# Kernel tuning notes

Measured on AMD Instinct MI355X. Metric: run time of the kernel, lower is better.

## Reference

```python
import jax, jax.numpy as jnp
import numpy as np

N_HEADS = 16


def setup_inputs() -> dict:
    key = jax.random.key(0)
    ks = jax.random.split(key, 5)
    B, S, L, E, H = 8, 2048, 512, 1024, 1024
    x = jax.random.normal(ks[0], (B, S, E), dtype=jnp.float32)
    latents = jax.random.normal(ks[1], (B, L, E), dtype=jnp.float32)
    mask_x = jnp.ones((B, S), dtype=jnp.float32)
    mask_latent = jnp.ones((B, L), dtype=jnp.float32)
    # torch Linear(in, out, bias=False) stores W as [out, in] and computes x @ W.T;
    # we store [in, out] so forward is x @ W. Scale like torch default init.
    Wq = jax.random.normal(ks[2], (E, H), dtype=jnp.float32) / np.sqrt(E)
    Wkv = jax.random.normal(ks[3], (E, 2 * H), dtype=jnp.float32) / np.sqrt(E)
    Wp = jax.random.normal(ks[4], (H, E), dtype=jnp.float32) / np.sqrt(H)
    return {"x": x, "latents": latents, "mask_x": mask_x,
            "mask_latent": mask_latent, "Wq": Wq, "Wkv": Wkv, "Wp": Wp}


def reference(x, latents, mask_x, mask_latent, Wq, Wkv, Wp):
    B, L, E = latents.shape
    H = Wq.shape[1]
    d = H // N_HEADS

    q = latents @ Wq                                  # [B, L, H]
    kv_input = jnp.concatenate((x, latents), axis=1)  # [B, S+L, E]
    kv_mask = jnp.concatenate((mask_x, mask_latent), axis=1)  # [B, S+L]
    kv = kv_input @ Wkv                               # [B, S+L, 2H]
    k, v = kv[..., :H], kv[..., H:]

    def heads(t):  # [B, T, H] -> [B, nh, T, d]
        return t.reshape(t.shape[0], t.shape[1], N_HEADS, d).transpose(0, 2, 1, 3)

    q, k, v = heads(q), heads(k), heads(v)

    scores = jnp.einsum('bhld,bhsd->bhls', q, k) / jnp.sqrt(jnp.asarray(d, q.dtype))
    # additive padding mask: (1 - q_mask*kv_mask) * finfo.min, broadcast over heads
    m = mask_latent[:, None, :, None] * kv_mask[:, None, None, :]  # [B,1,L,S+L]
    scores = scores + (1.0 - m) * jnp.finfo(scores.dtype).min
    attn = jax.nn.softmax(scores, axis=-1)            # dropout is identity (eval)

    y = jnp.einsum('bhls,bhsd->bhld', attn, v)        # [B, nh, L, d]
    y = y.transpose(0, 2, 1, 3).reshape(B, L, H)
    return y @ Wp                                     # [B, L, E]
```

## Files before the change

kernel.cpp:

```cpp
#include <hip/hip_runtime.h>
#include <stdint.h>

typedef unsigned short u16;
typedef __attribute__((ext_vector_type(8))) short short8;
typedef __attribute__((ext_vector_type(4))) float f32x4;
typedef __attribute__((ext_vector_type(16))) float f32x16;
typedef __attribute__((ext_vector_type(4))) unsigned short u16x4;

__device__ __forceinline__ u16 f2bf(float f) {
  uint32_t u = __float_as_uint(f);
  return (u16)((u + 0x7FFFu + ((u >> 16) & 1u)) >> 16);
}

__device__ __forceinline__ void gl2lds16(const u16* g, u16* l) {
  __builtin_amdgcn_global_load_lds(
      (const __attribute__((address_space(1))) unsigned int*)g,
      (__attribute__((address_space(3))) unsigned int*)l, 16, 0, 0);
}

__device__ __forceinline__ float exp2fast(float x) {
#if __has_builtin(__builtin_amdgcn_exp2f)
  return __builtin_amdgcn_exp2f(x);
#else
  return exp2f(x);
#endif
}

__device__ __forceinline__ unsigned int cvtpk(float lo, float hi) {
  unsigned int r;
  asm("v_cvt_pk_bf16_f32 %0, %1, %2" : "=v"(r) : "v"(lo), "v"(hi));
  return r;
}

__device__ __forceinline__ float halfmax(float x) {
  auto r = __builtin_amdgcn_permlane32_swap(__float_as_uint(x), __float_as_uint(x), false, false);
  return fmaxf(__uint_as_float(r[0]), __uint_as_float(r[1]));
}
__device__ __forceinline__ float halfadd(float x) {
  auto r = __builtin_amdgcn_permlane32_swap(__float_as_uint(x), __float_as_uint(x), false, false);
  return __uint_as_float(r[0]) + __uint_as_float(r[1]);
}

__global__ __launch_bounds__(256) void conv_kvin(const float* __restrict__ x,
                                                 const float* __restrict__ lat,
                                                 u16* __restrict__ kvin) {
  const int64_t total8 = (int64_t)20480 * 1024 / 8;
  for (int64_t i = (int64_t)blockIdx.x * 256 + threadIdx.x; i < total8;
       i += (int64_t)gridDim.x * 256) {
    const int64_t e0 = i * 8;
    const int row = (int)(e0 >> 10);
    const int col = (int)(e0 & 1023);
    const int b = row / 2560;
    const int t = row - b * 2560;
    const float* src = (t < 2048)
        ? (x + ((int64_t)b * 2048 + t) * 1024 + col)
        : (lat + ((int64_t)b * 512 + (t - 2048)) * 1024 + col);
    const float4 v0 = *(const float4*)src;
    const float4 v1 = *(const float4*)(src + 4);
    union { u16 s[8]; short8 v; } pk;
    pk.s[0] = f2bf(v0.x); pk.s[1] = f2bf(v0.y); pk.s[2] = f2bf(v0.z); pk.s[3] = f2bf(v0.w);
    pk.s[4] = f2bf(v1.x); pk.s[5] = f2bf(v1.y); pk.s[6] = f2bf(v1.z); pk.s[7] = f2bf(v1.w);
    *(short8*)(kvin + e0) = pk.v;
  }
}

__global__ __launch_bounds__(256) void prep_bias(const float* __restrict__ mask_x,
                                                 const float* __restrict__ mask_lat,
                                                 float* __restrict__ biasKV) {
  const int i = blockIdx.x * 256 + threadIdx.x;
  if (i >= 20480) return;
  const int b = i / 2560, t = i - b * 2560;
  const float m = (t < 2048) ? mask_x[b * 2048 + t] : mask_lat[b * 512 + t - 2048];
  biasKV[i] = (1.0f - m) * (-1.0e30f);
}

__global__ __launch_bounds__(256) void convT(const float* __restrict__ src,
                                             u16* __restrict__ dst, int K, int N) {
  __shared__ float tile[32][33];
  const int kb = blockIdx.x * 32, nb = blockIdx.y * 32;
  const int tx = threadIdx.x & 31, ty = threadIdx.x >> 5;
  #pragma unroll
  for (int i = 0; i < 4; i++)
    tile[ty + i * 8][tx] = src[(int64_t)(kb + ty + i * 8) * N + nb + tx];
  __syncthreads();
  #pragma unroll
  for (int i = 0; i < 4; i++)
    dst[(int64_t)(nb + ty + i * 8) * K + kb + tx] = f2bf(tile[tx][ty + i * 8]);
}

template <int MODE>
__global__ __launch_bounds__(256) void gemm128(const u16* __restrict__ A0,
                                               const u16* __restrict__ Bt,
                                               void* __restrict__ C0,
                                               void* __restrict__ C1) {
  __shared__ u16 As[128 * 64];
  __shared__ u16 Bs[128 * 64];
  const int tid = threadIdx.x;
  const int lane = tid & 63, wave = tid >> 6;
  const int l16 = lane & 15, g4 = lane >> 4;
  const int bm = blockIdx.x, bn = blockIdx.y;

  const u16* Arow;
  if (MODE == 0) {
    const int b = bm >> 2;
    Arow = A0 + ((int64_t)b * 2560 + 2048 + (int64_t)(bm & 3) * 128) * 1024;
  } else {
    Arow = A0 + (int64_t)bm * 128 * 1024;
  }
  const u16* Brow = Bt + (int64_t)bn * 128 * 1024;

  const int wm = wave >> 1, wn = wave & 1;
  const int sr = lane >> 3;
  const int ss = lane & 7;
  const int swslot = (ss ^ sr) * 8;

  f32x4 acc[4][4];
  #pragma unroll
  for (int m = 0; m < 4; m++)
    #pragma unroll
    for (int n = 0; n < 4; n++)
      acc[m][n] = (f32x4){0.f, 0.f, 0.f, 0.f};

  for (int kt = 0; kt < 1024; kt += 64) {
    #pragma unroll
    for (int i = 0; i < 4; i++) {
      const int c = wave * 4 + i;
      gl2lds16(Arow + (int64_t)(c * 8 + sr) * 1024 + kt + swslot, &As[c * 512]);
      gl2lds16(Brow + (int64_t)(c * 8 + sr) * 1024 + kt + swslot, &Bs[c * 512]);
    }
    __syncthreads();
    #pragma unroll
    for (int kk = 0; kk < 2; kk++) {
      short8 af[4], bfr[4];
      #pragma unroll
      for (int m = 0; m < 4; m++)
        af[m] = *(const short8*)&As[(wm * 64 + m * 16 + l16) * 64 +
                                    (((kk * 4 + g4) ^ (l16 & 7)) * 8)];
      #pragma unroll
      for (int n = 0; n < 4; n++)
        bfr[n] = *(const short8*)&Bs[(wn * 64 + n * 16 + l16) * 64 +
                                     (((kk * 4 + g4) ^ (l16 & 7)) * 8)];
      #pragma unroll
      for (int m = 0; m < 4; m++)
        #pragma unroll
        for (int n = 0; n < 4; n++)
          acc[m][n] = __builtin_amdgcn_mfma_f32_16x16x32_bf16(af[m], bfr[n], acc[m][n], 0, 0, 0);
    }
    __syncthreads();
  }

  const int g4e = lane >> 4;
  const int r0 = bm * 128 + wm * 64;
  const int c0 = bn * 128 + wn * 64;
  #pragma unroll
  for (int m = 0; m < 4; m++) {
    #pragma unroll
    for (int n = 0; n < 4; n++) {
      const int col = c0 + n * 16 + l16;
      if (MODE == 1 && col >= 1024) {
        const int rbase = r0 + m * 16 + g4e * 4;
        const int b = rbase / 2560;
        const int t = rbase - b * 2560;
        u16x4 vv;
        vv[0] = f2bf(acc[m][n][0]); vv[1] = f2bf(acc[m][n][1]);
        vv[2] = f2bf(acc[m][n][2]); vv[3] = f2bf(acc[m][n][3]);
        *(u16x4*)((u16*)C1 + ((int64_t)b * 1024 + (col - 1024)) * 2560 + t) = vv;
      } else {
        #pragma unroll
        for (int j = 0; j < 4; j++) {
          const int row = r0 + m * 16 + g4e * 4 + j;
          const float v = acc[m][n][j];
          if (MODE == 2)      ((float*)C0)[(int64_t)row * 1024 + col] = v;
          else if (MODE == 0) ((u16*)C0)[(int64_t)row * 1024 + col] = f2bf(v * 0.18033688f);
          else                ((u16*)C0)[(int64_t)row * 1024 + col] = f2bf(v);
        }
      }
    }
  }
}

__global__ __launch_bounds__(256, 2) void attn5(const u16* __restrict__ q,
                                                const u16* __restrict__ kbuf,
                                                const u16* __restrict__ vT,
                                                const float* __restrict__ biasKV,
                                                u16* __restrict__ y) {
  __shared__ u16 Klds[2][64][64];
  __shared__ u16 Vlds[2][64][64];

  const int id = blockIdx.x;
  const int xcd = id & 7, rest = id >> 3;
  const int bh = xcd * 16 + (rest >> 2);
  const int qb = rest & 3;
  const int b = bh >> 4, h = bh & 15;
  const int lane = threadIdx.x & 63, wave = threadIdx.x >> 6;
  const int l32 = lane & 31, hi = lane >> 5;
  const int q0 = qb * 128 + wave * 32;

  const u16* kg = kbuf + (int64_t)(b * 2560) * 1024 + h * 64;
  const u16* vg = vT + ((int64_t)(b * 1024 + h * 64)) * 2560;
  const float* bbase = biasKV + b * 2560;

  short8 qf[4];
  const u16* qrow = q + ((int64_t)(b * 512 + q0 + l32)) * 1024 + h * 64;
  #pragma unroll
  for (int c = 0; c < 4; c++)
    qf[c] = *(const short8*)(qrow + c * 16 + hi * 8);

  float mrun = -3.0e38f, lsum = 0.f;
  f32x16 yacc0, yacc1;
  #pragma unroll
  for (int i = 0; i < 16; i++) { yacc0[i] = 0.f; yacc1[i] = 0.f; }

  const int sr = lane >> 3;
  const int ss = lane & 7;
  const int swslot = (ss ^ sr) * 8;

  #pragma unroll
  for (int j = 0; j < 2; j++) {
    const int r = wave * 16 + j * 8 + sr;
    gl2lds16(kg + (int64_t)r * 1024 + swslot, &Klds[0][wave * 16 + j * 8][0]);
    gl2lds16(vg + (int64_t)r * 2560 + swslot, &Vlds[0][wave * 16 + j * 8][0]);
  }
  __syncthreads();

  int cur = 0;
  for (int tile = 0; tile < 40; ++tile) {
    const int T0 = tile * 64;
    if (tile + 1 < 40) {
      const int nb = cur ^ 1, T1 = T0 + 64;
      #pragma unroll
      for (int j = 0; j < 2; j++) {
        const int r = wave * 16 + j * 8 + sr;
        gl2lds16(kg + (int64_t)(T1 + r) * 1024 + swslot, &Klds[nb][wave * 16 + j * 8][0]);
        gl2lds16(vg + (int64_t)r * 2560 + T1 + swslot, &Vlds[nb][wave * 16 + j * 8][0]);
      }
    }

    #pragma unroll
    for (int ht = 0; ht < 2; ++ht) {
      const int t0h = T0 + ht * 32;
      short8 kf[4];
      #pragma unroll
      for (int c = 0; c < 4; c++)
        kf[c] = *(const short8*)&Klds[cur][ht * 32 + l32][((c * 2 + hi) ^ (l32 & 7)) * 8];
      short8 vf[2][2];
      #pragma unroll
      for (int db = 0; db < 2; db++)
        #pragma unroll
        for (int ks = 0; ks < 2; ks++)
          vf[db][ks] = *(const short8*)&Vlds[cur][db * 32 + l32]
                                            [((ht * 4 + ks * 2 + hi) ^ (l32 & 7)) * 8];
      float4 bb[4];
      #pragma unroll
      for (int g = 0; g < 4; g++)
        bb[g] = *(const float4*)(bbase + t0h + g * 8 + hi * 4);

      f32x16 S;
      #pragma unroll
      for (int i = 0; i < 16; i++) S[i] = 0.f;
      #pragma unroll
      for (int c = 0; c < 4; c++)
        S = __builtin_amdgcn_mfma_f32_32x32x16_bf16(kf[c], qf[c], S, 0, 0, 0);

      float t[16];
      #pragma unroll
      for (int r = 0; r < 16; r++) t[r] = S[r] + bb[r >> 2][r & 3];

      float m01 = fmaxf(t[0], t[1]),  m23 = fmaxf(t[2], t[3]);
      float m45 = fmaxf(t[4], t[5]),  m67 = fmaxf(t[6], t[7]);
      float m89 = fmaxf(t[8], t[9]),  mab = fmaxf(t[10], t[11]);
      float mcd = fmaxf(t[12], t[13]), mef = fmaxf(t[14], t[15]);
      float tm = fmaxf(fmaxf(fmaxf(m01, m23), fmaxf(m45, m67)),
                       fmaxf(fmaxf(m89, mab), fmaxf(mcd, mef)));
      tm = halfmax(tm);

      if (__any(tm > mrun + 8.f)) {
        const float nm = fmaxf(mrun, tm);
        const float alpha = exp2fast(mrun - nm);
        mrun = nm;
        lsum *= alpha;
        #pragma unroll
        for (int i = 0; i < 16; i++) { yacc0[i] *= alpha; yacc1[i] *= alpha; }
      }

      float p[16];
      #pragma unroll
      for (int r = 0; r < 16; r++) p[r] = exp2fast(t[r] - mrun);

      float ps = ((p[0] + p[1]) + (p[2] + p[3])) + ((p[4] + p[5]) + (p[6] + p[7]));
      ps += ((p[8] + p[9]) + (p[10] + p[11])) + ((p[12] + p[13]) + (p[14] + p[15]));
      lsum += halfadd(ps);

      union PA { unsigned int w[4]; short8 v; } pa0, pa1;
      {
        auto r0 = __builtin_amdgcn_permlane32_swap(cvtpk(p[0], p[1]), cvtpk(p[4], p[5]), false, false);
        pa0.w[0] = r0[0]; pa0.w[2] = r0[1];
        auto r1 = __builtin_amdgcn_permlane32_swap(cvtpk(p[2], p[3]), cvtpk(p[6], p[7]), false, false);
        pa0.w[1] = r1[0]; pa0.w[3] = r1[1];
        auto r2 = __builtin_amdgcn_permlane32_swap(cvtpk(p[8], p[9]), cvtpk(p[12], p[13]), false, false);
        pa1.w[0] = r2[0]; pa1.w[2] = r2[1];
        auto r3 = __builtin_amdgcn_permlane32_swap(cvtpk(p[10], p[11]), cvtpk(p[14], p[15]), false, false);
        pa1.w[1] = r3[0]; pa1.w[3] = r3[1];
      }

      yacc0 = __builtin_amdgcn_mfma_f32_32x32x16_bf16(vf[0][0], pa0.v, yacc0, 0, 0, 0);
      yacc0 = __builtin_amdgcn_mfma_f32_32x32x16_bf16(vf[0][1], pa1.v, yacc0, 0, 0, 0);
      yacc1 = __builtin_amdgcn_mfma_f32_32x32x16_bf16(vf[1][0], pa0.v, yacc1, 0, 0, 0);
      yacc1 = __builtin_amdgcn_mfma_f32_32x32x16_bf16(vf[1][1], pa1.v, yacc1, 0, 0, 0);
    }

    __syncthreads();
    cur ^= 1;
  }

  const float inv = 1.0f / lsum;
  u16* yr = y + ((int64_t)(b * 512 + q0 + l32)) * 1024 + h * 64;
  #pragma unroll
  for (int g = 0; g < 4; g++) {
    u16x4 o0, o1;
    #pragma unroll
    for (int j = 0; j < 4; j++) {
      o0[j] = f2bf(yacc0[g * 4 + j] * inv);
      o1[j] = f2bf(yacc1[g * 4 + j] * inv);
    }
    *(u16x4*)(yr + g * 8 + hi * 4) = o0;
    *(u16x4*)(yr + 32 + g * 8 + hi * 4) = o1;
  }
}

extern "C" void kernel_launch(void* const* d_in, const int* in_sizes, int n_in,
                              void* d_out, int out_size, void* d_ws, size_t ws_size,
                              hipStream_t stream) {
  const float* x        = (const float*)d_in[0];
  const float* lat      = (const float*)d_in[1];
  const float* mask_x   = (const float*)d_in[2];
  const float* mask_lat = (const float*)d_in[3];
  const float* Wq       = (const float*)d_in[4];
  const float* Wkv      = (const float*)d_in[5];
  const float* Wp       = (const float*)d_in[6];

  u16* kvin = (u16*)d_ws;
  u16* WqT  = kvin + (int64_t)20480 * 1024;
  u16* WkvT = WqT  + (int64_t)1024 * 1024;
  u16* WpT  = WkvT + (int64_t)2048 * 1024;
  u16* qb   = WpT  + (int64_t)1024 * 1024;
  u16* kb   = qb   + (int64_t)4096 * 1024;
  u16* vT   = kb   + (int64_t)20480 * 1024;
  float* biasKV = (float*)(vT + (int64_t)20480 * 1024);
  u16* yb   = kvin;

  conv_kvin<<<2560, 256, 0, stream>>>(x, lat, kvin);
  prep_bias<<<80, 256, 0, stream>>>(mask_x, mask_lat, biasKV);
  convT<<<dim3(32, 32), 256, 0, stream>>>(Wq, WqT, 1024, 1024);
  convT<<<dim3(32, 64), 256, 0, stream>>>(Wkv, WkvT, 1024, 2048);
  convT<<<dim3(32, 32), 256, 0, stream>>>(Wp, WpT, 1024, 1024);

  gemm128<0><<<dim3(32, 8), 256, 0, stream>>>(kvin, WqT, qb, nullptr);
  gemm128<1><<<dim3(160, 16), 256, 0, stream>>>(kvin, WkvT, kb, vT);
  attn5<<<512, 256, 0, stream>>>(qb, kb, vT, biasKV, yb);
  gemm128<2><<<dim3(32, 8), 256, 0, stream>>>(yb, WpT, d_out, nullptr);
}
```

Before: 365.2 us.

## Replace KV projection GEMM with 256x256 double-buffered 8-wave kernel

The KV projection, the largest GEMM (20480x2048x1024), moves from the 128x128 single-buffered kernel to a dedicated 256x256-tile, 512-thread kernel. It double-buffers LDS, interleaves the next tile's global-to-LDS loads with MFMA phases using explicit vmcnt waits and barriers, raises wave priority around the MFMAs, and remaps block IDs across XCDs for L2 locality. The aim is more data reuse per tile and hidden load latency. In exchange it uses more LDS and registers per block, and the hand-tuned waitcnt/barrier sequence is fragile.

```diff
diff --git a/kernel.cpp b/kernel.cpp
--- a/kernel.cpp
+++ b/kernel.cpp
@@ -91,8 +91,7 @@
 template <int MODE>
 __global__ __launch_bounds__(256) void gemm128(const u16* __restrict__ A0,
                                                const u16* __restrict__ Bt,
-                                               void* __restrict__ C0,
-                                               void* __restrict__ C1) {
+                                               void* __restrict__ C0) {
   __shared__ u16 As[128 * 64];
   __shared__ u16 Bs[128 * 64];
   const int tid = threadIdx.x;
@@ -149,7 +148,6 @@
     __syncthreads();
   }
 
-  const int g4e = lane >> 4;
   const int r0 = bm * 128 + wm * 64;
   const int c0 = bn * 128 + wn * 64;
   #pragma unroll
@@ -157,23 +155,142 @@
     #pragma unroll
     for (int n = 0; n < 4; n++) {
       const int col = c0 + n * 16 + l16;
-      if (MODE == 1 && col >= 1024) {
-        const int rbase = r0 + m * 16 + g4e * 4;
+      #pragma unroll
+      for (int j = 0; j < 4; j++) {
+        const int row = r0 + m * 16 + g4 * 4 + j;
+        const float v = acc[m][n][j];
+        if (MODE == 2)      ((float*)C0)[(int64_t)row * 1024 + col] = v;
+        else                ((u16*)C0)[(int64_t)row * 1024 + col] = f2bf(v * 0.18033688f);
+      }
+    }
+  }
+}
+
+__global__ __launch_bounds__(512, 2) void gemm256kv(const u16* __restrict__ A0,
+                                                    const u16* __restrict__ Bt,
+                                                    u16* __restrict__ kb,
+                                                    u16* __restrict__ vT) {
+  __shared__ u16 As[2][256][64];
+  __shared__ u16 Bs[2][256][64];
+  const int tid = threadIdx.x;
+  const int lane = tid & 63, wave = tid >> 6;
+  const int l16 = lane & 15, g4 = lane >> 4;
+  const int wm = wave >> 2, wn = wave & 3;
+
+  const int id = blockIdx.x;
+  const int wgid = (id & 7) * 80 + (id >> 3);
+  const int bm = wgid >> 3, bn = wgid & 7;
+
+  const u16* Arow = A0 + (int64_t)bm * 256 * 1024;
+  const u16* Brow = Bt + (int64_t)bn * 256 * 1024;
+
+  const int sr = lane >> 3;
+  const int ss = lane & 7;
+  const int swslot = (ss ^ sr) * 8;
+  const int g8 = wave * 8;
+
+  f32x4 acc[8][4];
+  #pragma unroll
+  for (int m = 0; m < 8; m++)
+    #pragma unroll
+    for (int n = 0; n < 4; n++)
+      acc[m][n] = (f32x4){0.f, 0.f, 0.f, 0.f};
+
+  {
+    const int kt = 0;
+    #pragma unroll
+    for (int c = 0; c < 4; c++)
+      gl2lds16(Brow + (int64_t)(c * 64 + g8 + sr) * 1024 + kt + swslot, &Bs[0][c * 64 + g8][0]);
+    gl2lds16(Arow + (int64_t)(0 * 64 + g8 + sr) * 1024 + kt + swslot, &As[0][0 * 64 + g8][0]);
+    gl2lds16(Arow + (int64_t)(2 * 64 + g8 + sr) * 1024 + kt + swslot, &As[0][2 * 64 + g8][0]);
+    gl2lds16(Arow + (int64_t)(1 * 64 + g8 + sr) * 1024 + kt + swslot, &As[0][1 * 64 + g8][0]);
+    gl2lds16(Arow + (int64_t)(3 * 64 + g8 + sr) * 1024 + kt + swslot, &As[0][3 * 64 + g8][0]);
+  }
+
+  for (int t = 0; t < 16; ++t) {
+    const int buf = t & 1, nb = buf ^ 1;
+    const int ktn = (t + 1) * 64;
+    const bool more = (t + 1 < 16);
+    short8 bf[4][2];
+
+    #pragma unroll
+    for (int q = 0; q < 4; ++q) {
+      if (q == 0) {
+        asm volatile("s_waitcnt vmcnt(2)" ::: "memory");
+        __builtin_amdgcn_s_barrier();
+      }
+      if (q == 2) {
+        if (more) asm volatile("s_waitcnt vmcnt(4)" ::: "memory");
+        else      asm volatile("s_waitcnt vmcnt(0)" ::: "memory");
+        __builtin_amdgcn_s_barrier();
+      }
+
+      if (q == 0) {
+        #pragma unroll
+        for (int n = 0; n < 4; n++)
+          #pragma unroll
+          for (int kk = 0; kk < 2; kk++)
+            bf[n][kk] = *(const short8*)&Bs[buf][wn * 64 + n * 16 + l16]
+                                            [((kk * 4 + g4) ^ (l16 & 7)) * 8];
+      }
+      short8 af[2][2];
+      #pragma unroll
+      for (int m2 = 0; m2 < 2; m2++)
+        #pragma unroll
+        for (int kk = 0; kk < 2; kk++)
+          af[m2][kk] = *(const short8*)&As[buf][wm * 128 + (q * 2 + m2) * 16 + l16]
+                                          [((kk * 4 + g4) ^ (l16 & 7)) * 8];
+
+      if (more) {
+        if (q == 0) {
+          gl2lds16(Brow + (int64_t)(0 * 64 + g8 + sr) * 1024 + ktn + swslot, &Bs[nb][0 * 64 + g8][0]);
+          gl2lds16(Brow + (int64_t)(1 * 64 + g8 + sr) * 1024 + ktn + swslot, &Bs[nb][1 * 64 + g8][0]);
+        } else if (q == 1) {
+          gl2lds16(Brow + (int64_t)(2 * 64 + g8 + sr) * 1024 + ktn + swslot, &Bs[nb][2 * 64 + g8][0]);
+          gl2lds16(Brow + (int64_t)(3 * 64 + g8 + sr) * 1024 + ktn + swslot, &Bs[nb][3 * 64 + g8][0]);
+        } else if (q == 2) {
+          gl2lds16(Arow + (int64_t)(0 * 64 + g8 + sr) * 1024 + ktn + swslot, &As[nb][0 * 64 + g8][0]);
+          gl2lds16(Arow + (int64_t)(2 * 64 + g8 + sr) * 1024 + ktn + swslot, &As[nb][2 * 64 + g8][0]);
+        } else {
+          gl2lds16(Arow + (int64_t)(1 * 64 + g8 + sr) * 1024 + ktn + swslot, &As[nb][1 * 64 + g8][0]);
+          gl2lds16(Arow + (int64_t)(3 * 64 + g8 + sr) * 1024 + ktn + swslot, &As[nb][3 * 64 + g8][0]);
+        }
+      }
+
+      __builtin_amdgcn_s_barrier();
+      __builtin_amdgcn_s_setprio(1);
+      #pragma unroll
+      for (int m2 = 0; m2 < 2; m2++)
+        #pragma unroll
+        for (int n = 0; n < 4; n++)
+          #pragma unroll
+          for (int kk = 0; kk < 2; kk++)
+            acc[q * 2 + m2][n] = __builtin_amdgcn_mfma_f32_16x16x32_bf16(
+                af[m2][kk], bf[n][kk], acc[q * 2 + m2][n], 0, 0, 0);
+      __builtin_amdgcn_s_setprio(0);
+      __builtin_amdgcn_s_barrier();
+    }
+  }
+
+  const int r0 = bm * 256 + wm * 128;
+  const int c0 = bn * 256 + wn * 64;
+  #pragma unroll
+  for (int m = 0; m < 8; m++) {
+    #pragma unroll
+    for (int n = 0; n < 4; n++) {
+      const int col = c0 + n * 16 + l16;
+      const int rbase = r0 + m * 16 + g4 * 4;
+      if (col >= 1024) {
         const int b = rbase / 2560;
         const int t = rbase - b * 2560;
         u16x4 vv;
         vv[0] = f2bf(acc[m][n][0]); vv[1] = f2bf(acc[m][n][1]);
         vv[2] = f2bf(acc[m][n][2]); vv[3] = f2bf(acc[m][n][3]);
-        *(u16x4*)((u16*)C1 + ((int64_t)b * 1024 + (col - 1024)) * 2560 + t) = vv;
+        *(u16x4*)(vT + ((int64_t)b * 1024 + (col - 1024)) * 2560 + t) = vv;
       } else {
         #pragma unroll
-        for (int j = 0; j < 4; j++) {
-          const int row = r0 + m * 16 + g4e * 4 + j;
-          const float v = acc[m][n][j];
-          if (MODE == 2)      ((float*)C0)[(int64_t)row * 1024 + col] = v;
-          else if (MODE == 0) ((u16*)C0)[(int64_t)row * 1024 + col] = f2bf(v * 0.18033688f);
-          else                ((u16*)C0)[(int64_t)row * 1024 + col] = f2bf(v);
-        }
+        for (int j = 0; j < 4; j++)
+          kb[(int64_t)(rbase + j) * 1024 + col] = f2bf(acc[m][n][j]);
       }
     }
   }
@@ -355,8 +472,8 @@
   convT<<<dim3(32, 64), 256, 0, stream>>>(Wkv, WkvT, 1024, 2048);
   convT<<<dim3(32, 32), 256, 0, stream>>>(Wp, WpT, 1024, 1024);
 
-  gemm128<0><<<dim3(32, 8), 256, 0, stream>>>(kvin, WqT, qb, nullptr);
-  gemm128<1><<<dim3(160, 16), 256, 0, stream>>>(kvin, WkvT, kb, vT);
+  gemm128<0><<<dim3(32, 8), 256, 0, stream>>>(kvin, WqT, qb);
+  gemm256kv<<<640, 512, 0, stream>>>(kvin, WkvT, kb, vT);
   attn5<<<512, 256, 0, stream>>>(qb, kb, vT, biasKV, yb);
-  gemm128<2><<<dim3(32, 8), 256, 0, stream>>>(yb, WpT, d_out, nullptr);
-}
+  gemm128<2><<<dim3(32, 8), 256, 0, stream>>>(yb, WpT, d_out);
+}
```

New measurement: 362.5 us. About the same (-0.8%).
